# Kernel tuning notes

Measured on AMD Instinct MI355X. Metric: run time of the kernel, lower is better.

Reference implementation:

```python
import jax, jax.numpy as jnp
import numpy as np

N_CELLS = 200_000
N_FACES = 400_000
N_POINTS = 200_000
E_CF = 800_000
E_FP = 800_000
E_PP = 1_200_000
IN_C, IN_F, HID, OUT = 8, 8, 64, 128


def setup_inputs() -> dict:
    key = jax.random.key(0)
    ks = jax.random.split(key, 18)
    return {
        "x_centers": jax.random.normal(ks[0], (N_CELLS, IN_C), jnp.float32),
        "x_face": jax.random.normal(ks[1], (N_FACES, IN_F), jnp.float32),
        "W_cf": jax.random.normal(ks[2], (IN_C, HID), jnp.float32) * 0.1,
        "b_cf": jax.random.normal(ks[3], (HID,), jnp.float32) * 0.1,
        "W_fp": jax.random.normal(ks[4], (HID + IN_F, OUT), jnp.float32) * 0.1,
        "b_fp": jax.random.normal(ks[5], (OUT,), jnp.float32) * 0.1,
        "W_pp": jax.random.normal(ks[6], (OUT, OUT), jnp.float32) * 0.1,
        "W_pp_root": jax.random.normal(ks[7], (OUT, OUT), jnp.float32) * 0.1,
        "b_pp": jax.random.normal(ks[8], (OUT,), jnp.float32) * 0.1,
        "ea_cf": jax.random.uniform(ks[9], (E_CF,), jnp.float32),
        "ea_fp": jax.random.uniform(ks[10], (E_FP,), jnp.float32),
        "ea_pp": jax.random.uniform(ks[11], (E_PP,), jnp.float32),
        "src_cf": jax.random.randint(ks[12], (E_CF,), 0, N_CELLS, jnp.int32),
        "dst_cf": jax.random.randint(ks[13], (E_CF,), 0, N_FACES, jnp.int32),
        "src_fp": jax.random.randint(ks[14], (E_FP,), 0, N_FACES, jnp.int32),
        "dst_fp": jax.random.randint(ks[15], (E_FP,), 0, N_POINTS, jnp.int32),
        "src_pp": jax.random.randint(ks[16], (E_PP,), 0, N_POINTS, jnp.int32),
        "dst_pp": jax.random.randint(ks[17], (E_PP,), 0, N_POINTS, jnp.int32),
    }


def _graph_conv(x, W, b, src, dst, ea, n_dst):
    # transform-then-gather (small in-dim GEMM first), weight by edge_attr, scatter-sum
    h = x @ W                                   # [n_src, out]
    msg = h[src] * ea[:, None]                  # [E, out]
    return jax.ops.segment_sum(msg, dst, num_segments=n_dst) + b


def reference(x_centers, x_face, W_cf, b_cf, W_fp, b_fp, W_pp, W_pp_root, b_pp,
              ea_cf, ea_fp, ea_pp, src_cf, dst_cf, src_fp, dst_fp, src_pp, dst_pp):
    # layerCenterFace: cells -> faces
    y_face = _graph_conv(x_centers, W_cf, b_cf, src_cf, dst_cf, ea_cf, N_FACES)
    # concat learned face features with raw face features
    x = jnp.concatenate([y_face, x_face], axis=-1)          # [N_FACES, 72]
    # layerFacePoint: faces -> points
    y_pt = _graph_conv(x, W_fp, b_fp, src_fp, dst_fp, ea_fp, N_POINTS)
    # layerPointPoint: points -> points with root/self term
    msg = (y_pt @ W_pp)[src_pp] * ea_pp[:, None]            # [E_PP, 128]
    agg = jax.ops.segment_sum(msg, dst_pp, num_segments=N_POINTS)
    return y_pt @ W_pp_root + agg + b_pp                    # [N_POINTS, 128]
```

## Files before the change

kernel.cpp:

```cpp
#include <hip/hip_runtime.h>
#include <hip/hip_bf16.h>

#define N_CELLS  200000
#define N_FACES  400000
#define N_POINTS 200000
#define E_CF     800000
#define E_FP     800000
#define E_PP     1200000
#define CAP_CF   16
#define CAP_FP   24
#define CAP_PP   32
#define OVF_CAP  4096
#define LDA96    104
#define LDA128   136

typedef __attribute__((ext_vector_type(8))) short bf16x8;
typedef __attribute__((ext_vector_type(8))) unsigned short u16x8;
typedef __attribute__((ext_vector_type(4))) float f32x4;

__device__ __forceinline__ float bf2f(unsigned short u) {
    union { unsigned int i; float f; } v; v.i = ((unsigned int)u) << 16; return v.f;
}
__device__ __forceinline__ unsigned short f2bf(float f) {
    __hip_bfloat16 h = __float2bfloat16(f);
    return *reinterpret_cast<unsigned short*>(&h);
}

__device__ __forceinline__ void fill_fixed(const int* __restrict__ src,
                                           const int* __restrict__ dst,
                                           const float* __restrict__ ea,
                                           int nE, int rlo, int rhi, int cap,
                                           int tid0, int stride,
                                           int* __restrict__ cnt,
                                           int2* __restrict__ pe,
                                           int* __restrict__ ovfn,
                                           int4* __restrict__ ovf) {
    for (int e = tid0; e < nE; e += stride) {
        int4 d4 = *(const int4*)(dst + e);
        int4 s4 = *(const int4*)(src + e);
        float4 w4 = *(const float4*)(ea + e);
        int dd[4] = {d4.x, d4.y, d4.z, d4.w};
        int ss[4] = {s4.x, s4.y, s4.z, s4.w};
        float ww[4] = {w4.x, w4.y, w4.z, w4.w};
#pragma unroll
        for (int i = 0; i < 4; ++i) {
            int d = dd[i];
            if (d >= rlo && d < rhi) {
                int t = atomicAdd(&cnt[d], 1);
                if (t < cap)
                    pe[(size_t)d * cap + t] = make_int2(ss[i], __float_as_int(ww[i]));
                else {
                    int g = atomicAdd(ovfn, 1);
                    if (g < OVF_CAP) ovf[g] = make_int4(d, ss[i], __float_as_int(ww[i]), 0);
                }
            }
        }
    }
}

__global__ __launch_bounds__(256) void k_fillA(const int* __restrict__ src_cf,
                                               const int* __restrict__ dst_cf,
                                               const float* __restrict__ ea_cf,
                                               int* __restrict__ cnt_cf,
                                               int2* __restrict__ pe_cf,
                                               const int* __restrict__ src_fp,
                                               const int* __restrict__ dst_fp,
                                               const float* __restrict__ ea_fp,
                                               int* __restrict__ cnt_fp,
                                               int2* __restrict__ pe_fp,
                                               int* __restrict__ ovfn,
                                               int4* __restrict__ ovf_cf,
                                               int4* __restrict__ ovf_fp,
                                               const float* __restrict__ W_fp,
                                               const float* __restrict__ W_rt,
                                               const float* __restrict__ W_pp,
                                               unsigned short* __restrict__ Bp_fp,
                                               unsigned short* __restrict__ Bp_fin) {
    int b = blockIdx.x;
    if (b < 512) {
        int p = b & 3;
        int blk = b >> 2;
        int rlo = p * 100000, rhi = rlo + 100000;
        int tid0 = (blk * 256 + (int)threadIdx.x) * 4;
        fill_fixed(src_cf, dst_cf, ea_cf, E_CF, rlo, rhi, CAP_CF,
                   tid0, 128 * 256 * 4, cnt_cf, pe_cf, ovfn, ovf_cf);
    } else if (b < 1024) {
        int bb = b - 512;
        int p = bb & 3;
        int blk = bb >> 2;
        int rlo = p * 50000, rhi = rlo + 50000;
        int tid0 = (blk * 256 + (int)threadIdx.x) * 4;
        fill_fixed(src_fp, dst_fp, ea_fp, E_FP, rlo, rhi, CAP_FP,
                   tid0, 128 * 256 * 4, cnt_fp, pe_fp, ovfn + 1, ovf_fp);
    } else if (b < 1072) {
        int t = (b - 1024) * 256 + threadIdx.x;
        int j = t & 7, lane = (t >> 3) & 63, ct = (t >> 9) & 7, ks = t >> 12;
        int k = ks * 32 + ((lane >> 4) & 3) * 8 + j;
        int col = ct * 16 + (lane & 15);
        Bp_fp[t] = f2bf(W_fp[k * 128 + col]);
    } else {
        int t = (b - 1072) * 256 + threadIdx.x;
        int j = t & 7, lane = (t >> 3) & 63, ct = (t >> 9) & 7, ks = t >> 12;
        int k = ks * 32 + ((lane >> 4) & 3) * 8 + j;
        int col = ct * 16 + (lane & 15);
        float v = (k < 128) ? W_rt[k * 128 + col] : W_pp[(k - 128) * 128 + col];
        Bp_fin[t] = f2bf(v);
    }
}

__global__ __launch_bounds__(256) void k_fillB(const int* __restrict__ src_pp,
                                               const int* __restrict__ dst_pp,
                                               const float* __restrict__ ea_pp,
                                               int* __restrict__ cnt_pp,
                                               int2* __restrict__ pe_pp,
                                               int* __restrict__ ovfn,
                                               int4* __restrict__ ovf_pp,
                                               const float* __restrict__ xc,
                                               const int* __restrict__ cnt_cf,
                                               const int2* __restrict__ pe_cf,
                                               const int* __restrict__ ovfn_cf,
                                               const int4* __restrict__ ovf_cf,
                                               const float* __restrict__ x_face,
                                               const float* __restrict__ W,
                                               const float* __restrict__ bvec,
                                               unsigned short* __restrict__ yfp) {
    __shared__ float Ws[512];
    __shared__ float bs[64];
    int b = blockIdx.x;
    if (b < 512) {
        int p = b & 3;
        int blk = b >> 2;
        int rlo = p * 50000, rhi = rlo + 50000;
        int tid0 = (blk * 256 + (int)threadIdx.x) * 4;
        fill_fixed(src_pp, dst_pp, ea_pp, E_PP, rlo, rhi, CAP_PP,
                   tid0, 128 * 256 * 4, cnt_pp, pe_pp, ovfn + 2, ovf_pp);
        return;
    }
    for (int i = threadIdx.x; i < 512; i += 256) Ws[i] = W[i];
    if (threadIdx.x < 64) bs[threadIdx.x] = bvec[threadIdx.x];
    __syncthreads();
    int r = (b - 512) * 256 + threadIdx.x;
    if (r >= N_FACES) return;
    int n = cnt_cf[r]; if (n > CAP_CF) n = CAP_CF;
    const int2* prow = pe_cf + (size_t)r * CAP_CF;
    float a[8] = {};
    int e = 0;
    for (; e + 1 < n; e += 2) {
        int2 q0 = prow[e], q1 = prow[e + 1];
        float w0 = __int_as_float(q0.y), w1 = __int_as_float(q1.y);
        const float* p0 = xc + (size_t)q0.x * 8;
        const float* p1 = xc + (size_t)q1.x * 8;
        float4 u0 = *(const float4*)p0, u1 = *(const float4*)(p0 + 4);
        float4 v0 = *(const float4*)p1, v1 = *(const float4*)(p1 + 4);
        a[0] += w0 * u0.x + w1 * v0.x; a[1] += w0 * u0.y + w1 * v0.y;
        a[2] += w0 * u0.z + w1 * v0.z; a[3] += w0 * u0.w + w1 * v0.w;
        a[4] += w0 * u1.x + w1 * v1.x; a[5] += w0 * u1.y + w1 * v1.y;
        a[6] += w0 * u1.z + w1 * v1.z; a[7] += w0 * u1.w + w1 * v1.w;
    }
    if (e < n) {
        int2 q0 = prow[e];
        float w0 = __int_as_float(q0.y);
        const float* p0 = xc + (size_t)q0.x * 8;
        float4 u0 = *(const float4*)p0, u1 = *(const float4*)(p0 + 4);
        a[0] += w0 * u0.x; a[1] += w0 * u0.y; a[2] += w0 * u0.z; a[3] += w0 * u0.w;
        a[4] += w0 * u1.x; a[5] += w0 * u1.y; a[6] += w0 * u1.z; a[7] += w0 * u1.w;
    }
    int no = *ovfn_cf;
    if (no > 0) {
        if (no > OVF_CAP) no = OVF_CAP;
        for (int i = 0; i < no; ++i) {
            int4 o = ovf_cf[i];
            if (o.x == r) {
                float w0 = __int_as_float(o.z);
                const float* p0 = xc + (size_t)o.y * 8;
#pragma unroll
                for (int k = 0; k < 8; ++k) a[k] += w0 * p0[k];
            }
        }
    }
    unsigned short* orow = yfp + (size_t)r * 96;
#pragma unroll
    for (int c4 = 0; c4 < 4; ++c4) {
        int j0 = c4 * 16;
        float acc[16];
#pragma unroll
        for (int i = 0; i < 16; ++i) acc[i] = bs[j0 + i];
#pragma unroll
        for (int k = 0; k < 8; ++k) {
            float x = a[k];
            const float* wr = Ws + k * 64 + j0;
#pragma unroll
            for (int i = 0; i < 16; ++i) acc[i] += x * wr[i];
        }
        u16x8 o0, o1;
#pragma unroll
        for (int i = 0; i < 8; ++i) { o0[i] = f2bf(acc[i]); o1[i] = f2bf(acc[8 + i]); }
        *(u16x8*)(orow + j0) = o0;
        *(u16x8*)(orow + j0 + 8) = o1;
    }
    float4 xf0 = *(const float4*)(x_face + (size_t)r * 8);
    float4 xf1 = *(const float4*)(x_face + (size_t)r * 8 + 4);
    u16x8 xo;
    xo[0] = f2bf(xf0.x); xo[1] = f2bf(xf0.y); xo[2] = f2bf(xf0.z); xo[3] = f2bf(xf0.w);
    xo[4] = f2bf(xf1.x); xo[5] = f2bf(xf1.y); xo[6] = f2bf(xf1.z); xo[7] = f2bf(xf1.w);
    *(u16x8*)(orow + 64) = xo;
}

__global__ __launch_bounds__(256) void k_g96_mfma(const unsigned short* __restrict__ feat,
                                                  const int* __restrict__ cnt,
                                                  const int2* __restrict__ pe,
                                                  const int* __restrict__ ovfn,
                                                  const int4* __restrict__ ovf,
                                                  const unsigned short* __restrict__ Bp,
                                                  const float* __restrict__ bias,
                                                  unsigned short* __restrict__ O) {
    __shared__ __align__(16) unsigned short Asub[32 * LDA96];
    const int w = threadIdx.x >> 6;
    const int lane = threadIdx.x & 63;
    const int l = lane & 31;
    const int R0 = blockIdx.x * 32;
    for (int rr = 0; rr < 4; ++rr) {
        int row = R0 + w * 8 + rr * 2 + (lane >> 5);
        int n = cnt[row]; if (n > CAP_FP) n = CAP_FP;
        const int2* prow = pe + (size_t)row * CAP_FP;
        float a0 = 0.f, a1 = 0.f, a2 = 0.f;
        int e = 0;
        for (; e + 3 < n; e += 4) {
            int2 q0 = prow[e], q1 = prow[e + 1], q2 = prow[e + 2], q3 = prow[e + 3];
            float w0 = __int_as_float(q0.y), w1 = __int_as_float(q1.y);
            float w2 = __int_as_float(q2.y), w3 = __int_as_float(q3.y);
            const unsigned short* f0 = feat + (size_t)q0.x * 96 + l;
            const unsigned short* f1 = feat + (size_t)q1.x * 96 + l;
            const unsigned short* f2 = feat + (size_t)q2.x * 96 + l;
            const unsigned short* f3 = feat + (size_t)q3.x * 96 + l;
            a0 += w0 * bf2f(f0[0])  + w1 * bf2f(f1[0])  + w2 * bf2f(f2[0])  + w3 * bf2f(f3[0]);
            a1 += w0 * bf2f(f0[32]) + w1 * bf2f(f1[32]) + w2 * bf2f(f2[32]) + w3 * bf2f(f3[32]);
            a2 += w0 * bf2f(f0[64]) + w1 * bf2f(f1[64]) + w2 * bf2f(f2[64]) + w3 * bf2f(f3[64]);
        }
        for (; e < n; ++e) {
            int2 q0 = prow[e];
            float w0 = __int_as_float(q0.y);
            const unsigned short* f0 = feat + (size_t)q0.x * 96 + l;
            a0 += w0 * bf2f(f0[0]); a1 += w0 * bf2f(f0[32]); a2 += w0 * bf2f(f0[64]);
        }
        int no = *ovfn;
        if (no > 0) {
            if (no > OVF_CAP) no = OVF_CAP;
            for (int i = 0; i < no; ++i) {
                int4 o = ovf[i];
                if (o.x == row) {
                    float w0 = __int_as_float(o.z);
                    const unsigned short* f0 = feat + (size_t)o.y * 96 + l;
                    a0 += w0 * bf2f(f0[0]); a1 += w0 * bf2f(f0[32]); a2 += w0 * bf2f(f0[64]);
                }
            }
        }
        int lr = row - R0;
        Asub[lr * LDA96 + l]      = f2bf(a0);
        Asub[lr * LDA96 + 32 + l] = f2bf(a1);
        Asub[lr * LDA96 + 64 + l] = f2bf(a2);
    }
    __syncthreads();
    const int rg = w >> 1, cg = w & 1;
    bf16x8 bfr[3][4];
#pragma unroll
    for (int ks = 0; ks < 3; ++ks)
#pragma unroll
        for (int c = 0; c < 4; ++c) {
            int ct = cg * 4 + c;
            bfr[ks][c] = *(const bf16x8*)(Bp + ((size_t)(ks * 8 + ct) * 64 + lane) * 8);
        }
    f32x4 acc[4] = {};
    const unsigned short* arow = Asub + (rg * 16 + (lane & 15)) * LDA96 + ((lane >> 4) * 8);
#pragma unroll
    for (int ks = 0; ks < 3; ++ks) {
        bf16x8 af = *(const bf16x8*)(arow + ks * 32);
#pragma unroll
        for (int c = 0; c < 4; ++c)
            acc[c] = __builtin_amdgcn_mfma_f32_16x16x32_bf16(af, bfr[ks][c], acc[c], 0, 0, 0);
    }
    const int row0 = R0 + rg * 16;
    const int rbase = row0 + (lane >> 4) * 4;
#pragma unroll
    for (int c = 0; c < 4; ++c) {
        int gcol = cg * 64 + c * 16 + (lane & 15);
        float bv = bias[gcol];
#pragma unroll
        for (int r = 0; r < 4; ++r)
            O[(size_t)(rbase + r) * 128 + gcol] = f2bf(acc[c][r] + bv);
    }
}

__global__ __launch_bounds__(256) void k_gpp_fin(const unsigned short* __restrict__ feat,
                                                 const int* __restrict__ cnt,
                                                 const int2* __restrict__ pe,
                                                 const int* __restrict__ ovfn,
                                                 const int4* __restrict__ ovf,
                                                 const unsigned short* __restrict__ A1,
                                                 const unsigned short* __restrict__ Bp,
                                                 const float* __restrict__ bias,
                                                 float* __restrict__ out) {
    __shared__ __align__(16) unsigned short Asub[32 * LDA128];
    const int w = threadIdx.x >> 6;
    const int lane = threadIdx.x & 63;
    const int l = lane & 31;
    const int R0 = blockIdx.x * 32;
    for (int rr = 0; rr < 4; ++rr) {
        int row = R0 + w * 8 + rr * 2 + (lane >> 5);
        int n = cnt[row]; if (n > CAP_PP) n = CAP_PP;
        const int2* prow = pe + (size_t)row * CAP_PP;
        float a0 = 0.f, a1 = 0.f, a2 = 0.f, a3 = 0.f;
        int e = 0;
        for (; e + 3 < n; e += 4) {
            int2 q0 = prow[e], q1 = prow[e + 1], q2 = prow[e + 2], q3 = prow[e + 3];
            float w0 = __int_as_float(q0.y), w1 = __int_as_float(q1.y);
            float w2 = __int_as_float(q2.y), w3 = __int_as_float(q3.y);
            const unsigned short* f0 = feat + ((size_t)q0.x << 7) + l;
            const unsigned short* f1 = feat + ((size_t)q1.x << 7) + l;
            const unsigned short* f2 = feat + ((size_t)q2.x << 7) + l;
            const unsigned short* f3 = feat + ((size_t)q3.x << 7) + l;
            a0 += w0 * bf2f(f0[0])  + w1 * bf2f(f1[0])  + w2 * bf2f(f2[0])  + w3 * bf2f(f3[0]);
            a1 += w0 * bf2f(f0[32]) + w1 * bf2f(f1[32]) + w2 * bf2f(f2[32]) + w3 * bf2f(f3[32]);
            a2 += w0 * bf2f(f0[64]) + w1 * bf2f(f1[64]) + w2 * bf2f(f2[64]) + w3 * bf2f(f3[64]);
            a3 += w0 * bf2f(f0[96]) + w1 * bf2f(f1[96]) + w2 * bf2f(f2[96]) + w3 * bf2f(f3[96]);
        }
        for (; e < n; ++e) {
            int2 q0 = prow[e];
            float w0 = __int_as_float(q0.y);
            const unsigned short* f0 = feat + ((size_t)q0.x << 7) + l;
            a0 += w0 * bf2f(f0[0]);  a1 += w0 * bf2f(f0[32]);
            a2 += w0 * bf2f(f0[64]); a3 += w0 * bf2f(f0[96]);
        }
        int no = *ovfn;
        if (no > 0) {
            if (no > OVF_CAP) no = OVF_CAP;
            for (int i = 0; i < no; ++i) {
                int4 o = ovf[i];
                if (o.x == row) {
                    float w0 = __int_as_float(o.z);
                    const unsigned short* f0 = feat + ((size_t)o.y << 7) + l;
                    a0 += w0 * bf2f(f0[0]);  a1 += w0 * bf2f(f0[32]);
                    a2 += w0 * bf2f(f0[64]); a3 += w0 * bf2f(f0[96]);
                }
            }
        }
        int lr = row - R0;
        Asub[lr * LDA128 + l]      = f2bf(a0);
        Asub[lr * LDA128 + 32 + l] = f2bf(a1);
        Asub[lr * LDA128 + 64 + l] = f2bf(a2);
        Asub[lr * LDA128 + 96 + l] = f2bf(a3);
    }
    __syncthreads();
    const int rg = w >> 1, cg = w & 1;
    bf16x8 bfr[8][4];
#pragma unroll
    for (int ks = 0; ks < 8; ++ks)
#pragma unroll
        for (int c = 0; c < 4; ++c) {
            int ct = cg * 4 + c;
            bfr[ks][c] = *(const bf16x8*)(Bp + ((size_t)(ks * 8 + ct) * 64 + lane) * 8);
        }
    f32x4 acc[4] = {};
    const unsigned short* a1p = A1 + (size_t)(R0 + rg * 16 + (lane & 15)) * 128 + ((lane >> 4) * 8);
    const unsigned short* a2p = Asub + (rg * 16 + (lane & 15)) * LDA128 + ((lane >> 4) * 8);
#pragma unroll
    for (int ks = 0; ks < 4; ++ks) {
        bf16x8 af = *(const bf16x8*)(a1p + ks * 32);
#pragma unroll
        for (int c = 0; c < 4; ++c)
            acc[c] = __builtin_amdgcn_mfma_f32_16x16x32_bf16(af, bfr[ks][c], acc[c], 0, 0, 0);
    }
#pragma unroll
    for (int ks = 0; ks < 4; ++ks) {
        bf16x8 af = *(const bf16x8*)(a2p + ks * 32);
#pragma unroll
        for (int c = 0; c < 4; ++c)
            acc[c] = __builtin_amdgcn_mfma_f32_16x16x32_bf16(af, bfr[ks + 4][c], acc[c], 0, 0, 0);
    }
    const int row0 = R0 + rg * 16;
    const int rbase = row0 + (lane >> 4) * 4;
#pragma unroll
    for (int c = 0; c < 4; ++c) {
        int gcol = cg * 64 + c * 16 + (lane & 15);
        float bv = bias[gcol];
#pragma unroll
        for (int r = 0; r < 4; ++r)
            out[(size_t)(rbase + r) * 128 + gcol] = acc[c][r] + bv;
    }
}

extern "C" void kernel_launch(void* const* d_in, const int* in_sizes, int n_in,
                              void* d_out, int out_size, void* d_ws, size_t ws_size,
                              hipStream_t stream) {
    const float* x_centers = (const float*)d_in[0];
    const float* x_face    = (const float*)d_in[1];
    const float* W_cf      = (const float*)d_in[2];
    const float* b_cf      = (const float*)d_in[3];
    const float* W_fp      = (const float*)d_in[4];
    const float* b_fp      = (const float*)d_in[5];
    const float* W_pp      = (const float*)d_in[6];
    const float* W_rt      = (const float*)d_in[7];
    const float* b_pp      = (const float*)d_in[8];
    const float* ea_cf     = (const float*)d_in[9];
    const float* ea_fp     = (const float*)d_in[10];
    const float* ea_pp     = (const float*)d_in[11];
    const int* src_cf      = (const int*)d_in[12];
    const int* dst_cf      = (const int*)d_in[13];
    const int* src_fp      = (const int*)d_in[14];
    const int* dst_fp      = (const int*)d_in[15];
    const int* src_pp      = (const int*)d_in[16];
    const int* dst_pp      = (const int*)d_in[17];
    float* out = (float*)d_out;

    char* ws = (char*)d_ws;
    unsigned short* yfp    = (unsigned short*)(ws + 0);
    unsigned short* y_ptb  = (unsigned short*)(ws + 80000000);
    int2* pe_fp            = (int2*)(ws + 132000000);
    int2* pe_cf            = (int2*)(ws + 172000000);
    int2* pe_pp            = (int2*)(ws + 224000000);
    int*  cnt_cf           = (int*)(ws + 280000000);
    int*  cnt_fp           = (int*)(ws + 281600000);
    int*  cnt_pp           = (int*)(ws + 282400000);
    int*  ovfn             = (int*)(ws + 283200000);
    int4* ovf_cf           = (int4*)(ws + 284000000);
    int4* ovf_fp           = (int4*)(ws + 284100000);
    int4* ovf_pp           = (int4*)(ws + 284200000);
    unsigned short* Bp_fp  = (unsigned short*)(ws + 284300000);
    unsigned short* Bp_fin = (unsigned short*)(ws + 284400000);

    hipMemsetAsync(cnt_cf, 0, 3200016, stream);
    k_fillA<<<1200, 256, 0, stream>>>(src_cf, dst_cf, ea_cf, cnt_cf, pe_cf,
                                      src_fp, dst_fp, ea_fp, cnt_fp, pe_fp,
                                      ovfn, ovf_cf, ovf_fp,
                                      W_fp, W_rt, W_pp, Bp_fp, Bp_fin);
    k_fillB<<<512 + 1563, 256, 0, stream>>>(src_pp, dst_pp, ea_pp, cnt_pp, pe_pp,
                                            ovfn, ovf_pp,
                                            x_centers, cnt_cf, pe_cf, ovfn, ovf_cf,
                                            x_face, W_cf, b_cf, yfp);
    k_g96_mfma<<<6250, 256, 0, stream>>>(yfp, cnt_fp, pe_fp, ovfn + 1, ovf_fp, Bp_fp, b_fp, y_ptb);
    k_gpp_fin<<<6250, 256, 0, stream>>>(y_ptb, cnt_pp, pe_pp, ovfn + 2, ovf_pp, y_ptb, Bp_fin, b_pp, out);
}
```

Before: 389.4 us.

## Fold cell-face weights into face-point GEMM and gather 17-wide features instead

The cell→face linear layer is folded algebraically into the face→point layer: W_cf@W_fp[:64] and b_cf@W_fp[:64] are precomputed into a 17x128 fp32 table (plus the x_face rows and b_fp). The face stage now stores only the 8-wide aggregated cell features in fp32, and the point stage gathers 8+8+1 values per edge instead of 96 bf16 values, then applies a small fp32 FMA GEMM. This removes the 96-wide face feature materialisation and most of the gather traffic, and swaps MFMA for scalar FMA on a much smaller K. The final output is also written with nontemporal stores.

```diff
diff --git a/kernel.cpp b/kernel.cpp
--- a/kernel.cpp
+++ b/kernel.cpp
@@ -11,7 +11,6 @@
 #define CAP_FP   24
 #define CAP_PP   32
 #define OVF_CAP  4096
-#define LDA96    104
 #define LDA128   136
 
 typedef __attribute__((ext_vector_type(8))) short bf16x8;
@@ -71,11 +70,16 @@
                                                int* __restrict__ ovfn,
                                                int4* __restrict__ ovf_cf,
                                                int4* __restrict__ ovf_fp,
+                                               const float* __restrict__ W_cf,
+                                               const float* __restrict__ b_cf,
                                                const float* __restrict__ W_fp,
+                                               const float* __restrict__ b_fp,
                                                const float* __restrict__ W_rt,
                                                const float* __restrict__ W_pp,
-                                               unsigned short* __restrict__ Bp_fp,
+                                               float* __restrict__ Wt,
                                                unsigned short* __restrict__ Bp_fin) {
+    __shared__ float WcfS[512];
+    __shared__ float bcfS[64];
     int b = blockIdx.x;
     if (b < 512) {
         int p = b & 3;
@@ -92,19 +96,36 @@
         int tid0 = (blk * 256 + (int)threadIdx.x) * 4;
         fill_fixed(src_fp, dst_fp, ea_fp, E_FP, rlo, rhi, CAP_FP,
                    tid0, 128 * 256 * 4, cnt_fp, pe_fp, ovfn + 1, ovf_fp);
-    } else if (b < 1072) {
+    } else if (b < 1152) {
         int t = (b - 1024) * 256 + threadIdx.x;
-        int j = t & 7, lane = (t >> 3) & 63, ct = (t >> 9) & 7, ks = t >> 12;
-        int k = ks * 32 + ((lane >> 4) & 3) * 8 + j;
-        int col = ct * 16 + (lane & 15);
-        Bp_fp[t] = f2bf(W_fp[k * 128 + col]);
-    } else {
-        int t = (b - 1072) * 256 + threadIdx.x;
         int j = t & 7, lane = (t >> 3) & 63, ct = (t >> 9) & 7, ks = t >> 12;
         int k = ks * 32 + ((lane >> 4) & 3) * 8 + j;
         int col = ct * 16 + (lane & 15);
         float v = (k < 128) ? W_rt[k * 128 + col] : W_pp[(k - 128) * 128 + col];
         Bp_fin[t] = f2bf(v);
+    } else {
+        for (int i = threadIdx.x; i < 512; i += 256) WcfS[i] = W_cf[i];
+        if (threadIdx.x < 64) bcfS[threadIdx.x] = b_cf[threadIdx.x];
+        __syncthreads();
+        int t = threadIdx.x;
+        int j = t & 127;
+        if (t < 128) {
+            float accW[8] = {};
+            float accb = 0.f;
+            for (int m = 0; m < 64; ++m) {
+                float wf = W_fp[m * 128 + j];
+#pragma unroll
+                for (int k = 0; k < 8; ++k) accW[k] += WcfS[k * 64 + m] * wf;
+                accb += bcfS[m] * wf;
+            }
+#pragma unroll
+            for (int k = 0; k < 8; ++k) Wt[k * 128 + j] = accW[k];
+            Wt[16 * 128 + j] = accb;
+        } else {
+#pragma unroll
+            for (int k = 0; k < 8; ++k) Wt[(8 + k) * 128 + j] = W_fp[(64 + k) * 128 + j];
+            Wt[17 * 128 + j] = b_fp[j];
+        }
     }
 }
 
@@ -120,12 +141,7 @@
                                                const int2* __restrict__ pe_cf,
                                                const int* __restrict__ ovfn_cf,
                                                const int4* __restrict__ ovf_cf,
-                                               const float* __restrict__ x_face,
-                                               const float* __restrict__ W,
-                                               const float* __restrict__ bvec,
-                                               unsigned short* __restrict__ yfp) {
-    __shared__ float Ws[512];
-    __shared__ float bs[64];
+                                               float* __restrict__ aggc) {
     int b = blockIdx.x;
     if (b < 512) {
         int p = b & 3;
@@ -136,9 +152,6 @@
                    tid0, 128 * 256 * 4, cnt_pp, pe_pp, ovfn + 2, ovf_pp);
         return;
     }
-    for (int i = threadIdx.x; i < 512; i += 256) Ws[i] = W[i];
-    if (threadIdx.x < 64) bs[threadIdx.x] = bvec[threadIdx.x];
-    __syncthreads();
     int r = (b - 512) * 256 + threadIdx.x;
     if (r >= N_FACES) return;
     int n = cnt_cf[r]; if (n > CAP_CF) n = CAP_CF;
@@ -178,70 +191,52 @@
             }
         }
     }
-    unsigned short* orow = yfp + (size_t)r * 96;
-#pragma unroll
-    for (int c4 = 0; c4 < 4; ++c4) {
-        int j0 = c4 * 16;
-        float acc[16];
-#pragma unroll
-        for (int i = 0; i < 16; ++i) acc[i] = bs[j0 + i];
-#pragma unroll
-        for (int k = 0; k < 8; ++k) {
-            float x = a[k];
-            const float* wr = Ws + k * 64 + j0;
-#pragma unroll
-            for (int i = 0; i < 16; ++i) acc[i] += x * wr[i];
-        }
-        u16x8 o0, o1;
-#pragma unroll
-        for (int i = 0; i < 8; ++i) { o0[i] = f2bf(acc[i]); o1[i] = f2bf(acc[8 + i]); }
-        *(u16x8*)(orow + j0) = o0;
-        *(u16x8*)(orow + j0 + 8) = o1;
-    }
-    float4 xf0 = *(const float4*)(x_face + (size_t)r * 8);
-    float4 xf1 = *(const float4*)(x_face + (size_t)r * 8 + 4);
-    u16x8 xo;
-    xo[0] = f2bf(xf0.x); xo[1] = f2bf(xf0.y); xo[2] = f2bf(xf0.z); xo[3] = f2bf(xf0.w);
-    xo[4] = f2bf(xf1.x); xo[5] = f2bf(xf1.y); xo[6] = f2bf(xf1.z); xo[7] = f2bf(xf1.w);
-    *(u16x8*)(orow + 64) = xo;
-}
-
-__global__ __launch_bounds__(256) void k_g96_mfma(const unsigned short* __restrict__ feat,
-                                                  const int* __restrict__ cnt,
-                                                  const int2* __restrict__ pe,
-                                                  const int* __restrict__ ovfn,
-                                                  const int4* __restrict__ ovf,
-                                                  const unsigned short* __restrict__ Bp,
-                                                  const float* __restrict__ bias,
-                                                  unsigned short* __restrict__ O) {
-    __shared__ __align__(16) unsigned short Asub[32 * LDA96];
-    const int w = threadIdx.x >> 6;
-    const int lane = threadIdx.x & 63;
-    const int l = lane & 31;
+    float4* o4 = (float4*)(aggc + (size_t)r * 8);
+    o4[0] = make_float4(a[0], a[1], a[2], a[3]);
+    o4[1] = make_float4(a[4], a[5], a[6], a[7]);
+}
+
+__global__ __launch_bounds__(256) void k_g17(const float* __restrict__ aggc,
+                                             const float* __restrict__ x_face,
+                                             const int* __restrict__ cnt,
+                                             const int2* __restrict__ pe,
+                                             const int* __restrict__ ovfn,
+                                             const int4* __restrict__ ovf,
+                                             const float* __restrict__ Wt,
+                                             unsigned short* __restrict__ y_ptb) {
+    __shared__ float A_s[32][18];
+    __shared__ float Wt_s[18 * 128];
+    for (int i = threadIdx.x; i < 18 * 128; i += 256) Wt_s[i] = Wt[i];
+    const int hw = threadIdx.x >> 5;
+    const int l = threadIdx.x & 31;
     const int R0 = blockIdx.x * 32;
-    for (int rr = 0; rr < 4; ++rr) {
-        int row = R0 + w * 8 + rr * 2 + (lane >> 5);
+    for (int pp = 0; pp < 4; ++pp) {
+        int row = R0 + hw * 4 + pp;
         int n = cnt[row]; if (n > CAP_FP) n = CAP_FP;
         const int2* prow = pe + (size_t)row * CAP_FP;
-        float a0 = 0.f, a1 = 0.f, a2 = 0.f;
+        float acc = 0.f;
         int e = 0;
         for (; e + 3 < n; e += 4) {
             int2 q0 = prow[e], q1 = prow[e + 1], q2 = prow[e + 2], q3 = prow[e + 3];
-            float w0 = __int_as_float(q0.y), w1 = __int_as_float(q1.y);
-            float w2 = __int_as_float(q2.y), w3 = __int_as_float(q3.y);
-            const unsigned short* f0 = feat + (size_t)q0.x * 96 + l;
-            const unsigned short* f1 = feat + (size_t)q1.x * 96 + l;
-            const unsigned short* f2 = feat + (size_t)q2.x * 96 + l;
-            const unsigned short* f3 = feat + (size_t)q3.x * 96 + l;
-            a0 += w0 * bf2f(f0[0])  + w1 * bf2f(f1[0])  + w2 * bf2f(f2[0])  + w3 * bf2f(f3[0]);
-            a1 += w0 * bf2f(f0[32]) + w1 * bf2f(f1[32]) + w2 * bf2f(f2[32]) + w3 * bf2f(f3[32]);
-            a2 += w0 * bf2f(f0[64]) + w1 * bf2f(f1[64]) + w2 * bf2f(f2[64]) + w3 * bf2f(f3[64]);
+#pragma unroll
+            for (int k = 0; k < 4; ++k) {
+                int2 q = (k == 0) ? q0 : (k == 1) ? q1 : (k == 2) ? q2 : q3;
+                float w = __int_as_float(q.y);
+                float v;
+                if (l < 8)       v = aggc[(size_t)q.x * 8 + l];
+                else if (l < 16) v = x_face[(size_t)q.x * 8 + (l - 8)];
+                else             v = (l == 16) ? 1.0f : 0.0f;
+                acc += w * v;
+            }
         }
         for (; e < n; ++e) {
-            int2 q0 = prow[e];
-            float w0 = __int_as_float(q0.y);
-            const unsigned short* f0 = feat + (size_t)q0.x * 96 + l;
-            a0 += w0 * bf2f(f0[0]); a1 += w0 * bf2f(f0[32]); a2 += w0 * bf2f(f0[64]);
+            int2 q = prow[e];
+            float w = __int_as_float(q.y);
+            float v;
+            if (l < 8)       v = aggc[(size_t)q.x * 8 + l];
+            else if (l < 16) v = x_face[(size_t)q.x * 8 + (l - 8)];
+            else             v = (l == 16) ? 1.0f : 0.0f;
+            acc += w * v;
         }
         int no = *ovfn;
         if (no > 0) {
@@ -249,46 +244,35 @@
             for (int i = 0; i < no; ++i) {
                 int4 o = ovf[i];
                 if (o.x == row) {
-                    float w0 = __int_as_float(o.z);
-                    const unsigned short* f0 = feat + (size_t)o.y * 96 + l;
-                    a0 += w0 * bf2f(f0[0]); a1 += w0 * bf2f(f0[32]); a2 += w0 * bf2f(f0[64]);
+                    float w = __int_as_float(o.z);
+                    float v;
+                    if (l < 8)       v = aggc[(size_t)o.y * 8 + l];
+                    else if (l < 16) v = x_face[(size_t)o.y * 8 + (l - 8)];
+                    else             v = (l == 16) ? 1.0f : 0.0f;
+                    acc += w * v;
                 }
             }
         }
-        int lr = row - R0;
-        Asub[lr * LDA96 + l]      = f2bf(a0);
-        Asub[lr * LDA96 + 32 + l] = f2bf(a1);
-        Asub[lr * LDA96 + 64 + l] = f2bf(a2);
+        if (l < 17) A_s[row - R0][l] = acc;
     }
     __syncthreads();
-    const int rg = w >> 1, cg = w & 1;
-    bf16x8 bfr[3][4];
-#pragma unroll
-    for (int ks = 0; ks < 3; ++ks)
-#pragma unroll
-        for (int c = 0; c < 4; ++c) {
-            int ct = cg * 4 + c;
-            bfr[ks][c] = *(const bf16x8*)(Bp + ((size_t)(ks * 8 + ct) * 64 + lane) * 8);
-        }
-    f32x4 acc[4] = {};
-    const unsigned short* arow = Asub + (rg * 16 + (lane & 15)) * LDA96 + ((lane >> 4) * 8);
-#pragma unroll
-    for (int ks = 0; ks < 3; ++ks) {
-        bf16x8 af = *(const bf16x8*)(arow + ks * 32);
-#pragma unroll
-        for (int c = 0; c < 4; ++c)
-            acc[c] = __builtin_amdgcn_mfma_f32_16x16x32_bf16(af, bfr[ks][c], acc[c], 0, 0, 0);
-    }
-    const int row0 = R0 + rg * 16;
-    const int rbase = row0 + (lane >> 4) * 4;
-#pragma unroll
-    for (int c = 0; c < 4; ++c) {
-        int gcol = cg * 64 + c * 16 + (lane & 15);
-        float bv = bias[gcol];
-#pragma unroll
-        for (int r = 0; r < 4; ++r)
-            O[(size_t)(rbase + r) * 128 + gcol] = f2bf(acc[c][r] + bv);
-    }
+    const int r = threadIdx.x >> 3;
+    const int jc = (threadIdx.x & 7) * 16;
+    float acc2[16];
+#pragma unroll
+    for (int i = 0; i < 16; ++i) acc2[i] = Wt_s[17 * 128 + jc + i];
+    for (int k = 0; k < 17; ++k) {
+        float av = A_s[r][k];
+        const float* wr = Wt_s + k * 128 + jc;
+#pragma unroll
+        for (int i = 0; i < 16; ++i) acc2[i] += av * wr[i];
+    }
+    u16x8 o0, o1;
+#pragma unroll
+    for (int i = 0; i < 8; ++i) { o0[i] = f2bf(acc2[i]); o1[i] = f2bf(acc2[8 + i]); }
+    unsigned short* orow = y_ptb + (size_t)(R0 + r) * 128 + jc;
+    *(u16x8*)orow = o0;
+    *(u16x8*)(orow + 8) = o1;
 }
 
 __global__ __launch_bounds__(256) void k_gpp_fin(const unsigned short* __restrict__ feat,
@@ -385,7 +369,8 @@
         float bv = bias[gcol];
 #pragma unroll
         for (int r = 0; r < 4; ++r)
-            out[(size_t)(rbase + r) * 128 + gcol] = acc[c][r] + bv;
+            __builtin_nontemporal_store(acc[c][r] + bv,
+                                        &out[(size_t)(rbase + r) * 128 + gcol]);
     }
 }
 
@@ -413,11 +398,12 @@
     float* out = (float*)d_out;
 
     char* ws = (char*)d_ws;
-    unsigned short* yfp    = (unsigned short*)(ws + 0);
-    unsigned short* y_ptb  = (unsigned short*)(ws + 80000000);
-    int2* pe_fp            = (int2*)(ws + 132000000);
-    int2* pe_cf            = (int2*)(ws + 172000000);
-    int2* pe_pp            = (int2*)(ws + 224000000);
+    float* aggc            = (float*)(ws + 0);
+    unsigned short* y_ptb  = (unsigned short*)(ws + 16000000);
+    float* Wt              = (float*)(ws + 68000000);
+    int2* pe_fp            = (int2*)(ws + 70000000);
+    int2* pe_cf            = (int2*)(ws + 110000000);
+    int2* pe_pp            = (int2*)(ws + 162000000);
     int*  cnt_cf           = (int*)(ws + 280000000);
     int*  cnt_fp           = (int*)(ws + 281600000);
     int*  cnt_pp           = (int*)(ws + 282400000);
@@ -425,18 +411,19 @@
     int4* ovf_cf           = (int4*)(ws + 284000000);
     int4* ovf_fp           = (int4*)(ws + 284100000);
     int4* ovf_pp           = (int4*)(ws + 284200000);
-    unsigned short* Bp_fp  = (unsigned short*)(ws + 284300000);
     unsigned short* Bp_fin = (unsigned short*)(ws + 284400000);
 
     hipMemsetAsync(cnt_cf, 0, 3200016, stream);
-    k_fillA<<<1200, 256, 0, stream>>>(src_cf, dst_cf, ea_cf, cnt_cf, pe_cf,
+    k_fillA<<<1153, 256, 0, stream>>>(src_cf, dst_cf, ea_cf, cnt_cf, pe_cf,
                                       src_fp, dst_fp, ea_fp, cnt_fp, pe_fp,
                                       ovfn, ovf_cf, ovf_fp,
-                                      W_fp, W_rt, W_pp, Bp_fp, Bp_fin);
+                                      W_cf, b_cf, W_fp, b_fp, W_rt, W_pp,
+                                      Wt, Bp_fin);
     k_fillB<<<512 + 1563, 256, 0, stream>>>(src_pp, dst_pp, ea_pp, cnt_pp, pe_pp,
                                             ovfn, ovf_pp,
                                             x_centers, cnt_cf, pe_cf, ovfn, ovf_cf,
-                                            x_face, W_cf, b_cf, yfp);
-    k_g96_mfma<<<6250, 256, 0, stream>>>(yfp, cnt_fp, pe_fp, ovfn + 1, ovf_fp, Bp_fp, b_fp, y_ptb);
-    k_gpp_fin<<<6250, 256, 0, stream>>>(y_ptb, cnt_pp, pe_pp, ovfn + 2, ovf_pp, y_ptb, Bp_fin, b_pp, out);
-}
+                                            aggc);
+    k_g17<<<6250, 256, 0, stream>>>(aggc, x_face, cnt_fp, pe_fp, ovfn + 1, ovf_fp, Wt, y_ptb);
+    k_gpp_fin<<<6250, 256, 0, stream>>>(y_ptb, cnt_pp, pe_pp, ovfn + 2, ovf_pp,
+                                        y_ptb, Bp_fin, b_pp, out);
+}
```

After: 429.0 us. +10.2%, slower.
